# Performance work log

Measured on AMD Instinct MI355X. Metric: run time of the kernel, lower is better.

Reference implementation:

```python
import jax, jax.numpy as jnp
import numpy as np

EPS = 1e-6

def rmsnorm(x, g):
    return x * jax.lax.rsqrt(jnp.mean(x * x, axis=-1, keepdims=True) + EPS) * g


def setup_inputs() -> dict:
    key = jax.random.key(0)
    B, T, D = 4, 4096, 1024
    ks = jax.random.split(key, 4)
    x = jax.random.normal(ks[0], (B, T, D), jnp.float32)
    W = jax.random.normal(ks[1], (B, D, D), jnp.float32) * 0.02  # recurrent state carry
    g_norm = jnp.ones((D,), jnp.float32)                          # RMSNorm gain
    Wp_w = jax.random.normal(ks[2], (D, D), jnp.float32) * (D ** -0.5)  # proj_w weight
    Wp_r = jax.random.normal(ks[3], (D, D), jnp.float32) * (D ** -0.5)  # proj_r weight
    decay = jnp.asarray(4.6, jnp.float32)                         # learned decay logit
    return {"x": x, "W": W, "g_norm": g_norm, "Wp_w": Wp_w, "Wp_r": Wp_r, "decay": decay}


def reference(x, W, g_norm, Wp_w, Wp_r, decay):
    B, T, D = x.shape
    # MambaBlock source unavailable: treated as identity, so out = RMSNorm(x)
    out = rmsnorm(x, g_norm)
    lg = jnp.log(jax.nn.sigmoid(decay))          # log-decay (negative scalar)
    v = out @ Wp_w.T                             # [B,T,D] values
    wk = jnp.pad(out[:, :-1], ((0, 0), (1, 0), (0, 0)))  # shift right by one step
    pos = jnp.arange(T)
    # exp-decay causal mask: exp(clamp(i-1-j,0)*lg) * (i>j)
    M = jnp.exp(jnp.maximum(pos[:, None] - 1 - pos[None, :], 0).astype(x.dtype) * lg)
    M = M * (pos[:, None] > pos[None, :]).astype(x.dtype)
    scores = jnp.einsum('btd,bsd->bts', out, wk) * M   # [B,T,T]
    reads = jnp.einsum('bts,bsd->btd', scores, v)      # [B,T,D]
    # recurrent-state read
    carry = jnp.einsum('bij,btj->bti', W, out)
    reads = reads + carry * jnp.exp(pos.astype(x.dtype) * lg)[None, :, None]
    # state update: w_t = exp((T-1-t)*lg)
    w = jnp.exp(jnp.arange(T - 1, -1, -1).astype(x.dtype) * lg)
    W_new = jnp.einsum('t,btd,bte->bde', w, v, wk) + jnp.exp(jnp.asarray(T, x.dtype) * lg) * W
    y = x + out + 0.03 * (reads @ Wp_r.T)
    return (y, W_new)
```

## Files before the change

### kernel.cpp

```cpp
#include <hip/hip_runtime.h>
#include <hip/hip_bf16.h>
#include <math.h>


typedef __hip_bfloat16 bf16;
typedef short bf16x8 __attribute__((ext_vector_type(8)));
typedef float f32x4 __attribute__((ext_vector_type(4)));

#define TPB 256
#define LC 10
#define CH (1 << LC)

__device__ __forceinline__ void gload_lds16(const void* g, void* l) {
  __builtin_amdgcn_global_load_lds(
      (const __attribute__((address_space(1))) unsigned int*)g,
      (__attribute__((address_space(3))) unsigned int*)l, 16, 0, 0);
}

enum { E_BF = 0, E_SCORES, E_READS, E_R1, E_FINAL };

struct MGP {
  const bf16 *A, *B;
  float *Cf; bf16 *Cb;
  const float *X; const bf16 *O;
  const float *dec;
  int K;
  int lda, ldb, ldc;
  long sAb, sBb, sCfb, sCbb, sOb, sCkb;
  int NC, aOff0, aStep, bOff0, bStep;
  int tri;
};

template<int MODE>
__global__ __launch_bounds__(TPB) void mg_k(MGP p) {
  __shared__ __align__(16) char ldsA[128 * 64 * 2];
  __shared__ __align__(16) char ldsB[128 * 64 * 2];
  const int tid = threadIdx.x;
  const int lane = tid & 63;
  const int w = tid >> 6;
  const int wr = w >> 1, wc = w & 1;
  const int z = blockIdx.z;
  const int b = z / p.NC, ch = z - b * p.NC;
  const int m0 = blockIdx.x * 128, n0 = blockIdx.y * 128;
  if constexpr (MODE == E_SCORES) {
    if (n0 > m0) return;
  }
  const float lg = -log1pf(expf(-p.dec[0]));
  const bf16* Ab = p.A + b * p.sAb + ((long)(p.aOff0 + ch * p.aStep) + m0) * p.lda;
  const bf16* Bb = p.B + b * p.sBb + ((long)(p.bOff0 + ch * p.bStep) + n0) * p.ldb;

  f32x4 acc[4][4];
#pragma unroll
  for (int i = 0; i < 4; i++)
#pragma unroll
    for (int j = 0; j < 4; j++) acc[i][j] = (f32x4){0.f, 0.f, 0.f, 0.f};

  const int Kend = p.tri ? (m0 + 128 < p.K ? m0 + 128 : p.K) : p.K;
  for (int k0 = 0; k0 < Kend; k0 += 64) {
#pragma unroll
    for (int c = 0; c < 4; c++) {
      const int o = w * 1024 + c * 4096 + lane * 16;
      const int row = o >> 7;
      const int cols = ((o & 127) ^ ((row & 7) << 4)) >> 1;
      gload_lds16(Ab + (long)row * p.lda + k0 + cols, ldsA + w * 1024 + c * 4096);
      gload_lds16(Bb + (long)row * p.ldb + k0 + cols, ldsB + w * 1024 + c * 4096);
    }
    __syncthreads();
#pragma unroll
    for (int ks = 0; ks < 2; ks++) {
      bf16x8 af[4], bfr[4];
      const int cB = ks * 64 + ((lane >> 4) << 4);
#pragma unroll
      for (int f = 0; f < 4; f++) {
        const int rA = wr * 64 + f * 16 + (lane & 15);
        af[f] = *(const bf16x8*)(ldsA + rA * 128 + (cB ^ ((rA & 7) << 4)));
        const int rB = wc * 64 + f * 16 + (lane & 15);
        bfr[f] = *(const bf16x8*)(ldsB + rB * 128 + (cB ^ ((rB & 7) << 4)));
      }
#pragma unroll
      for (int fm = 0; fm < 4; fm++)
#pragma unroll
        for (int fn = 0; fn < 4; fn++)
          acc[fm][fn] = __builtin_amdgcn_mfma_f32_16x16x32_bf16(af[fm], bfr[fn], acc[fm][fn], 0, 0, 0);
    }
    __syncthreads();
  }

#pragma unroll
  for (int fm = 0; fm < 4; fm++) {
#pragma unroll
    for (int fn = 0; fn < 4; fn++) {
#pragma unroll
      for (int r = 0; r < 4; r++) {
        const int m = m0 + wr * 64 + fm * 16 + ((lane >> 4) << 2) + r;
        const int n = n0 + wc * 64 + fn * 16 + (lane & 15);
        const float vacc = acc[fm][fn][r];
        if constexpr (MODE == E_BF) {
          p.Cb[b * p.sCbb + (long)m * p.ldc + n] = __float2bfloat16(vacc);
        } else if constexpr (MODE == E_SCORES) {
          const float sv = (n < m) ? vacc * __expf(lg * (float)(m - 1 - n)) : 0.f;
          p.Cb[b * p.sCbb + ch * p.sCkb + (long)m * p.ldc + n] = __float2bfloat16(sv);
        } else if constexpr (MODE == E_READS) {
          p.Cb[b * p.sCbb + ch * p.sCkb + (long)m * p.ldc + n] = __float2bfloat16(vacc);
        } else if constexpr (MODE == E_R1) {
          bf16* c = p.Cb + b * p.sCbb + ch * p.sCkb + (long)m * p.ldc + n;
          *c = __float2bfloat16(__bfloat162float(*c) + __expf(lg * (float)m) * vacc);
        } else {
          const long idx = b * p.sCfb + (long)m * p.ldc + n;
          const float ov = __bfloat162float(p.O[b * p.sOb + (long)(m + 1) * p.ldc + n]);
          p.Cf[idx] = p.X[idx] + ov + 0.03f * vacc;
        }
      }
    }
  }
}

__global__ __launch_bounds__(256) void rmsnorm_k(const float* __restrict__ x,
                                                 const float* __restrict__ g,
                                                 bf16* __restrict__ out_pad, int D, int T) {
  const long row = blockIdx.x;
  const long b = row / T, t = row - b * T;
  const float* xr = x + row * (long)D;
  bf16* orow = out_pad + (b * (long)(T + 1) + t + 1) * D;
  const int tid = threadIdx.x;
  const float4 xv = *(const float4*)&xr[tid * 4];
  float ss = xv.x * xv.x + xv.y * xv.y + xv.z * xv.z + xv.w * xv.w;
  for (int off = 32; off; off >>= 1) ss += __shfl_down(ss, off);
  __shared__ float sred[4];
  if ((tid & 63) == 0) sred[tid >> 6] = ss;
  __syncthreads();
  const float tot = sred[0] + sred[1] + sred[2] + sred[3];
  const float scale = rsqrtf(tot / (float)D + 1e-6f);
  const float4 gv = *(const float4*)&g[tid * 4];
  bf16 o4[4];
  o4[0] = __float2bfloat16(xv.x * scale * gv.x);
  o4[1] = __float2bfloat16(xv.y * scale * gv.y);
  o4[2] = __float2bfloat16(xv.z * scale * gv.z);
  o4[3] = __float2bfloat16(xv.w * scale * gv.w);
  *(ushort4*)(orow + tid * 4) = *(ushort4*)o4;
}

__global__ __launch_bounds__(256) void zpad_k(bf16* __restrict__ out_pad, int D, int T) {
  bf16* r = out_pad + (long)blockIdx.x * (T + 1) * D;
  ((ushort4*)r)[threadIdx.x] = make_ushort4(0, 0, 0, 0);
}

__global__ __launch_bounds__(256) void f2bf_k(const float* __restrict__ s, bf16* __restrict__ d, long n) {
  const long i = ((long)blockIdx.x * 256 + threadIdx.x) * 4;
  if (i >= n) return;
  const float4 v = *(const float4*)(s + i);
  bf16 o4[4] = {__float2bfloat16(v.x), __float2bfloat16(v.y),
                __float2bfloat16(v.z), __float2bfloat16(v.w)};
  *(ushort4*)(d + i) = *(ushort4*)o4;
}

__device__ __forceinline__ float4 load_bf4(const bf16* p) {
  const ushort4 u = *(const ushort4*)p;
  float4 f;
  f.x = __bfloat162float(*(const bf16*)&u.x);
  f.y = __bfloat162float(*(const bf16*)&u.y);
  f.z = __bfloat162float(*(const bf16*)&u.z);
  f.w = __bfloat162float(*(const bf16*)&u.w);
  return f;
}
__device__ __forceinline__ void store_bf4(bf16* p, float4 f) {
  bf16 o4[4] = {__float2bfloat16(f.x), __float2bfloat16(f.y),
                __float2bfloat16(f.z), __float2bfloat16(f.w)};
  *(ushort4*)p = *(ushort4*)o4;
}

__global__ __launch_bounds__(256) void comb_k(const float* __restrict__ W,
                                              const bf16* __restrict__ P,
                                              bf16* __restrict__ Sch,
                                              float* __restrict__ Wn,
                                              const float* __restrict__ dec,
                                              long DDl, int NC) {
  const long i = ((long)blockIdx.x * 256 + threadIdx.x) * 4;
  const int b = (int)(i / DDl);
  const long e = i - (long)b * DDl;
  const float lg = -log1pf(expf(-dec[0]));
  const float a = __expf(lg * (float)CH);
  float4 s = *(const float4*)(W + i);
  store_bf4(Sch + ((long)b * NC) * DDl + e, s);
  for (int ch = 0; ch < NC; ch++) {
    const float4 pp = load_bf4(P + ((long)b * NC + ch) * DDl + e);
    s.x = a * s.x + pp.x;  s.y = a * s.y + pp.y;
    s.z = a * s.z + pp.z;  s.w = a * s.w + pp.w;
    if (ch + 1 < NC) store_bf4(Sch + ((long)b * NC + ch + 1) * DDl + e, s);
  }
  *(float4*)(Wn + i) = s;
}

template<int WK>
__global__ __launch_bounds__(256) void tr_k(const bf16* __restrict__ src, bf16* __restrict__ dst,
                                            const float* __restrict__ dec, int D, int T, int NC) {
  __shared__ bf16 tl[32][33];
  const int b = blockIdx.z, d0 = blockIdx.x * 32, tg0 = blockIdx.y * 32;
  const int tx = threadIdx.x, ty = threadIdx.y;
  const float lg = -log1pf(expf(-dec[0]));
  for (int i = ty; i < 32; i += 8) {
    const int tg = tg0 + i;
    float val;
    if (WK)
      val = __expf(lg * (float)(CH - 1 - (tg & (CH - 1)))) *
            __bfloat162float(src[((long)b * (T + 1) + tg) * D + d0 + tx]);
    else
      val = __bfloat162float(src[((long)b * T + tg) * D + d0 + tx]);
    tl[i][tx] = __float2bfloat16(val);
  }
  __syncthreads();
  const int ch = tg0 >> LC, tc0 = tg0 & (CH - 1);
  for (int i = ty; i < 32; i += 8)
    dst[(((long)b * NC + ch) * D + d0 + i) * CH + tc0 + tx] = tl[tx][i];
}

extern "C" void kernel_launch(void* const* d_in, const int* in_sizes, int n_in,
                              void* d_out, int out_size, void* d_ws, size_t ws_size,
                              hipStream_t stream) {
  const float* x     = (const float*)d_in[0];
  const float* W     = (const float*)d_in[1];
  const float* g     = (const float*)d_in[2];
  const float* Wpw   = (const float*)d_in[3];
  const float* Wpr   = (const float*)d_in[4];
  const float* decay = (const float*)d_in[5];

  const int D  = in_sizes[2];
  const int Bn = in_sizes[1] / (D * D);
  const int T  = in_sizes[0] / (Bn * D);
  const int NC = T / CH;
  const long TD = (long)T * D, DD = (long)D * D, PD = (long)(T + 1) * D;

  bf16* out_pad  = (bf16*)d_ws;
  bf16* vT       = out_pad + Bn * PD;
  bf16* wkTw     = vT + Bn * TD;
  bf16* scores   = wkTw + Bn * TD;
  bf16* P_bf     = scores + (long)Bn * NC * CH * CH;
  bf16* Wpw_bf   = P_bf + (long)Bn * NC * DD;
  bf16* Wpr_bf   = Wpw_bf + DD;
  bf16* reads_bf = Wpr_bf + DD;
  bf16* v_rm     = scores;
  bf16* Sch      = scores;

  float* y = (float*)d_out;
  float* S = y + Bn * TD;

  rmsnorm_k<<<Bn * T, D / 4, 0, stream>>>(x, g, out_pad, D, T);
  zpad_k<<<Bn, 256, 0, stream>>>(out_pad, D, T);
  f2bf_k<<<(int)(DD / 1024), 256, 0, stream>>>(Wpw, Wpw_bf, DD);
  f2bf_k<<<(int)(DD / 1024), 256, 0, stream>>>(Wpr, Wpr_bf, DD);

  {
    MGP p{}; p.dec = decay;
    p.A = out_pad; p.lda = D; p.sAb = PD; p.aOff0 = 1;
    p.B = Wpw_bf;  p.ldb = D;
    p.Cb = v_rm; p.ldc = D; p.sCbb = TD;
    p.K = D; p.NC = 1;
    mg_k<E_BF><<<dim3(T / 128, D / 128, Bn), TPB, 0, stream>>>(p);
  }
  tr_k<0><<<dim3(D / 32, T / 32, Bn), dim3(32, 8), 0, stream>>>(v_rm, vT, decay, D, T, NC);
  tr_k<1><<<dim3(D / 32, T / 32, Bn), dim3(32, 8), 0, stream>>>(out_pad, wkTw, decay, D, T, NC);
  {
    MGP p{}; p.dec = decay;
    p.A = vT;   p.lda = CH; p.sAb = TD; p.aStep = D;
    p.B = wkTw; p.ldb = CH; p.sBb = TD; p.bStep = D;
    p.Cb = P_bf; p.ldc = D; p.sCbb = (long)NC * DD; p.sCkb = DD;
    p.K = CH; p.NC = NC;
    mg_k<E_READS><<<dim3(D / 128, D / 128, Bn * NC), TPB, 0, stream>>>(p);
  }
  {
    MGP p{}; p.dec = decay;
    p.A = out_pad; p.lda = D; p.sAb = PD; p.aOff0 = 1; p.aStep = CH;
    p.B = out_pad; p.ldb = D; p.sBb = PD; p.bOff0 = 0; p.bStep = CH;
    p.Cb = scores; p.ldc = CH; p.sCbb = (long)NC * CH * CH; p.sCkb = (long)CH * CH;
    p.K = D; p.NC = NC;
    mg_k<E_SCORES><<<dim3(CH / 128, CH / 128, Bn * NC), TPB, 0, stream>>>(p);
  }
  {
    MGP p{}; p.dec = decay;
    p.A = scores; p.lda = CH; p.sAb = (long)NC * CH * CH; p.aStep = CH;
    p.B = vT;     p.ldb = CH; p.sBb = TD; p.bStep = D;
    p.Cb = reads_bf; p.ldc = D; p.sCbb = TD; p.sCkb = (long)CH * D;
    p.K = CH; p.NC = NC; p.tri = 1;
    mg_k<E_READS><<<dim3(CH / 128, D / 128, Bn * NC), TPB, 0, stream>>>(p);
  }
  comb_k<<<(int)(Bn * DD / 1024), 256, 0, stream>>>(W, P_bf, Sch, S, decay, DD, NC);
  {
    MGP p{}; p.dec = decay;
    p.A = out_pad; p.lda = D; p.sAb = PD; p.aOff0 = 1; p.aStep = CH;
    p.B = Sch;     p.ldb = D; p.sBb = (long)NC * DD; p.bStep = D;
    p.Cb = reads_bf; p.ldc = D; p.sCbb = TD; p.sCkb = (long)CH * D;
    p.K = D; p.NC = NC;
    mg_k<E_R1><<<dim3(CH / 128, D / 128, Bn * NC), TPB, 0, stream>>>(p);
  }
  {
    MGP p{}; p.dec = decay;
    p.A = reads_bf; p.lda = D; p.sAb = TD;
    p.B = Wpr_bf;   p.ldb = D;
    p.Cf = y; p.ldc = D; p.sCfb = TD;
    p.X = x; p.O = out_pad; p.sOb = PD;
    p.K = D; p.NC = 1;
    mg_k<E_FINAL><<<dim3(T / 128, D / 128, Bn), TPB, 0, stream>>>(p);
  }
}
```

Before: 595.0 us.

## Fuse carry-read GEMM into reads GEMM and double-buffer LDS K loop

The inner GEMM loop changes from single-buffered 64-wide K tiles to a double-buffered pipeline of 32-wide K tiles, so the next tile's global-to-LDS load overlaps with MFMA work on the current one. The separate carry-read kernel, which read and rewrote reads_bf in bf16, is merged into the reads kernel. That kernel first accumulates out·Sch, scales it per row by exp(m·lg), then adds scores·vT in the same accumulators. This requires moving comb_k earlier and putting Sch in the wkTw buffer so it does not alias scores. The change removes one launch and a bf16 read-modify-write pass, at the cost of more register and scheduling pressure and a longer fused kernel.

```diff
diff --git a/kernel.cpp b/kernel.cpp
--- a/kernel.cpp
+++ b/kernel.cpp
@@ -17,24 +17,70 @@
       (__attribute__((address_space(3))) unsigned int*)l, 16, 0, 0);
 }
 
-enum { E_BF = 0, E_SCORES, E_READS, E_R1, E_FINAL };
+enum { E_BF = 0, E_SCORES, E_P, E_RDF, E_FINAL };
 
 struct MGP {
   const bf16 *A, *B;
+  const bf16 *A2, *B2;
   float *Cf; bf16 *Cb;
   const float *X; const bf16 *O;
   const float *dec;
-  int K;
-  int lda, ldb, ldc;
-  long sAb, sBb, sCfb, sCbb, sOb, sCkb;
-  int NC, aOff0, aStep, bOff0, bStep;
-  int tri;
+  int K, K2;
+  int lda, ldb, lda2, ldb2, ldc;
+  long sAb, sBb, sA2b, sB2b, sCfb, sCbb, sOb, sCkb;
+  int NC, aOff0, aStep, bOff0, bStep, a2Off0, a2Step, b2Step;
 };
+
+__device__ __forceinline__ void stage32(const bf16* Ab, int lda, const bf16* Bb, int ldb,
+                                        int k0, char* lA, char* lB, int w, int lane) {
+#pragma unroll
+  for (int c = 0; c < 2; c++) {
+    const int o = c * 4096 + w * 1024 + lane * 16;
+    const int row = o >> 6;
+    const int cols = ((o & 63) ^ (((row >> 1) & 3) << 4)) >> 1;
+    gload_lds16(Ab + (long)row * lda + k0 + cols, lA + c * 4096 + w * 1024);
+    gload_lds16(Bb + (long)row * ldb + k0 + cols, lB + c * 4096 + w * 1024);
+  }
+}
+
+__device__ __forceinline__ void comp32(const char* lA, const char* lB,
+                                       int wr, int wc, int lane, f32x4 (&acc)[4][4]) {
+  bf16x8 af[4], bfr[4];
+  const int j = lane >> 4;
+#pragma unroll
+  for (int f = 0; f < 4; f++) {
+    const int rA = wr * 64 + f * 16 + (lane & 15);
+    af[f] = *(const bf16x8*)(lA + rA * 64 + ((j ^ ((rA >> 1) & 3)) << 4));
+    const int rB = wc * 64 + f * 16 + (lane & 15);
+    bfr[f] = *(const bf16x8*)(lB + rB * 64 + ((j ^ ((rB >> 1) & 3)) << 4));
+  }
+#pragma unroll
+  for (int fm = 0; fm < 4; fm++)
+#pragma unroll
+    for (int fn = 0; fn < 4; fn++)
+      acc[fm][fn] = __builtin_amdgcn_mfma_f32_16x16x32_bf16(af[fm], bfr[fn], acc[fm][fn], 0, 0, 0);
+}
+
+__device__ __forceinline__ void gemm_pipe(const bf16* Ab, int lda, const bf16* Bb, int ldb,
+                                          int Kend, char* ldsA, char* ldsB,
+                                          int w, int lane, int wr, int wc, f32x4 (&acc)[4][4]) {
+  stage32(Ab, lda, Bb, ldb, 0, ldsA, ldsB, w, lane);
+  __syncthreads();
+  const int NT = Kend >> 5;
+  for (int t = 0; t < NT; t += 2) {
+    stage32(Ab, lda, Bb, ldb, (t + 1) * 32, ldsA + 8192, ldsB + 8192, w, lane);
+    comp32(ldsA, ldsB, wr, wc, lane, acc);
+    __syncthreads();
+    if (t + 2 < NT) stage32(Ab, lda, Bb, ldb, (t + 2) * 32, ldsA, ldsB, w, lane);
+    comp32(ldsA + 8192, ldsB + 8192, wr, wc, lane, acc);
+    __syncthreads();
+  }
+}
 
 template<int MODE>
 __global__ __launch_bounds__(TPB) void mg_k(MGP p) {
-  __shared__ __align__(16) char ldsA[128 * 64 * 2];
-  __shared__ __align__(16) char ldsB[128 * 64 * 2];
+  __shared__ __align__(16) char ldsA[2 * 8192];
+  __shared__ __align__(16) char ldsB[2 * 8192];
   const int tid = threadIdx.x;
   const int lane = tid & 63;
   const int w = tid >> 6;
@@ -46,8 +92,6 @@
     if (n0 > m0) return;
   }
   const float lg = -log1pf(expf(-p.dec[0]));
-  const bf16* Ab = p.A + b * p.sAb + ((long)(p.aOff0 + ch * p.aStep) + m0) * p.lda;
-  const bf16* Bb = p.B + b * p.sBb + ((long)(p.bOff0 + ch * p.bStep) + n0) * p.ldb;
 
   f32x4 acc[4][4];
 #pragma unroll
@@ -55,35 +99,26 @@
 #pragma unroll
     for (int j = 0; j < 4; j++) acc[i][j] = (f32x4){0.f, 0.f, 0.f, 0.f};
 
-  const int Kend = p.tri ? (m0 + 128 < p.K ? m0 + 128 : p.K) : p.K;
-  for (int k0 = 0; k0 < Kend; k0 += 64) {
-#pragma unroll
-    for (int c = 0; c < 4; c++) {
-      const int o = w * 1024 + c * 4096 + lane * 16;
-      const int row = o >> 7;
-      const int cols = ((o & 127) ^ ((row & 7) << 4)) >> 1;
-      gload_lds16(Ab + (long)row * p.lda + k0 + cols, ldsA + w * 1024 + c * 4096);
-      gload_lds16(Bb + (long)row * p.ldb + k0 + cols, ldsB + w * 1024 + c * 4096);
-    }
-    __syncthreads();
-#pragma unroll
-    for (int ks = 0; ks < 2; ks++) {
-      bf16x8 af[4], bfr[4];
-      const int cB = ks * 64 + ((lane >> 4) << 4);
-#pragma unroll
-      for (int f = 0; f < 4; f++) {
-        const int rA = wr * 64 + f * 16 + (lane & 15);
-        af[f] = *(const bf16x8*)(ldsA + rA * 128 + (cB ^ ((rA & 7) << 4)));
-        const int rB = wc * 64 + f * 16 + (lane & 15);
-        bfr[f] = *(const bf16x8*)(ldsB + rB * 128 + (cB ^ ((rB & 7) << 4)));
+  if constexpr (MODE == E_RDF) {
+    const bf16* A2 = p.A2 + b * p.sA2b + ((long)(p.a2Off0 + ch * p.a2Step) + m0) * p.lda2;
+    const bf16* B2 = p.B2 + b * p.sB2b + ((long)(ch * p.b2Step) + n0) * p.ldb2;
+    gemm_pipe(A2, p.lda2, B2, p.ldb2, p.K2, ldsA, ldsB, w, lane, wr, wc, acc);
+#pragma unroll
+    for (int fm = 0; fm < 4; fm++)
+#pragma unroll
+      for (int r = 0; r < 4; r++) {
+        const int mrow = m0 + wr * 64 + fm * 16 + ((lane >> 4) << 2) + r;
+        const float sc = __expf(lg * (float)mrow);
+#pragma unroll
+        for (int fn = 0; fn < 4; fn++) acc[fm][fn][r] *= sc;
       }
-#pragma unroll
-      for (int fm = 0; fm < 4; fm++)
-#pragma unroll
-        for (int fn = 0; fn < 4; fn++)
-          acc[fm][fn] = __builtin_amdgcn_mfma_f32_16x16x32_bf16(af[fm], bfr[fn], acc[fm][fn], 0, 0, 0);
-    }
-    __syncthreads();
+  }
+
+  {
+    const bf16* Ab = p.A + b * p.sAb + ((long)(p.aOff0 + ch * p.aStep) + m0) * p.lda;
+    const bf16* Bb = p.B + b * p.sBb + ((long)(p.bOff0 + ch * p.bStep) + n0) * p.ldb;
+    const int Kend = (MODE == E_RDF) ? (m0 + 128 < p.K ? m0 + 128 : p.K) : p.K;
+    gemm_pipe(Ab, p.lda, Bb, p.ldb, Kend, ldsA, ldsB, w, lane, wr, wc, acc);
   }
 
 #pragma unroll
@@ -100,11 +135,10 @@
         } else if constexpr (MODE == E_SCORES) {
           const float sv = (n < m) ? vacc * __expf(lg * (float)(m - 1 - n)) : 0.f;
           p.Cb[b * p.sCbb + ch * p.sCkb + (long)m * p.ldc + n] = __float2bfloat16(sv);
-        } else if constexpr (MODE == E_READS) {
+        } else if constexpr (MODE == E_P) {
           p.Cb[b * p.sCbb + ch * p.sCkb + (long)m * p.ldc + n] = __float2bfloat16(vacc);
-        } else if constexpr (MODE == E_R1) {
-          bf16* c = p.Cb + b * p.sCbb + ch * p.sCkb + (long)m * p.ldc + n;
-          *c = __float2bfloat16(__bfloat162float(*c) + __expf(lg * (float)m) * vacc);
+        } else if constexpr (MODE == E_RDF) {
+          p.Cb[b * p.sCbb + ch * p.sCkb + (long)m * p.ldc + n] = __float2bfloat16(vacc);
         } else {
           const long idx = b * p.sCfb + (long)m * p.ldc + n;
           const float ov = __bfloat162float(p.O[b * p.sOb + (long)(m + 1) * p.ldc + n]);
@@ -239,7 +273,7 @@
   bf16* Wpr_bf   = Wpw_bf + DD;
   bf16* reads_bf = Wpr_bf + DD;
   bf16* v_rm     = scores;
-  bf16* Sch      = scores;
+  bf16* Sch      = wkTw;
 
   float* y = (float*)d_out;
   float* S = y + Bn * TD;
@@ -265,8 +299,9 @@
     p.B = wkTw; p.ldb = CH; p.sBb = TD; p.bStep = D;
     p.Cb = P_bf; p.ldc = D; p.sCbb = (long)NC * DD; p.sCkb = DD;
     p.K = CH; p.NC = NC;
-    mg_k<E_READS><<<dim3(D / 128, D / 128, Bn * NC), TPB, 0, stream>>>(p);
-  }
+    mg_k<E_P><<<dim3(D / 128, D / 128, Bn * NC), TPB, 0, stream>>>(p);
+  }
+  comb_k<<<(int)(Bn * DD / 1024), 256, 0, stream>>>(W, P_bf, Sch, S, decay, DD, NC);
   {
     MGP p{}; p.dec = decay;
     p.A = out_pad; p.lda = D; p.sAb = PD; p.aOff0 = 1; p.aStep = CH;
@@ -277,20 +312,14 @@
   }
   {
     MGP p{}; p.dec = decay;
+    p.A2 = out_pad; p.lda2 = D; p.sA2b = PD; p.a2Off0 = 1; p.a2Step = CH;
+    p.B2 = Sch;     p.ldb2 = D; p.sB2b = (long)NC * DD; p.b2Step = D;
+    p.K2 = D;
     p.A = scores; p.lda = CH; p.sAb = (long)NC * CH * CH; p.aStep = CH;
     p.B = vT;     p.ldb = CH; p.sBb = TD; p.bStep = D;
     p.Cb = reads_bf; p.ldc = D; p.sCbb = TD; p.sCkb = (long)CH * D;
-    p.K = CH; p.NC = NC; p.tri = 1;
-    mg_k<E_READS><<<dim3(CH / 128, D / 128, Bn * NC), TPB, 0, stream>>>(p);
-  }
-  comb_k<<<(int)(Bn * DD / 1024), 256, 0, stream>>>(W, P_bf, Sch, S, decay, DD, NC);
-  {
-    MGP p{}; p.dec = decay;
-    p.A = out_pad; p.lda = D; p.sAb = PD; p.aOff0 = 1; p.aStep = CH;
-    p.B = Sch;     p.ldb = D; p.sBb = (long)NC * DD; p.bStep = D;
-    p.Cb = reads_bf; p.ldc = D; p.sCbb = TD; p.sCkb = (long)CH * D;
-    p.K = D; p.NC = NC;
-    mg_k<E_R1><<<dim3(CH / 128, D / 128, Bn * NC), TPB, 0, stream>>>(p);
+    p.K = CH; p.NC = NC;
+    mg_k<E_RDF><<<dim3(CH / 128, D / 128, Bn * NC), TPB, 0, stream>>>(p);
   }
   {
     MGP p{}; p.dec = decay;
```

Result: slower. 615.3 us (+3.4%).
